# Performance work log

Measured on AMD Instinct MI355X. Metric: run time of the kernel, lower is better.

Reference implementation:

```python
import jax, jax.numpy as jnp
import numpy as np

H = 64  # hidden_dim


def _gru_cell(x, h, W_ih, W_hh, b_ih, b_hh):
    # PyTorch GRU gate order: reset (r), update (z), new (n)
    gx = x @ W_ih.T + b_ih            # [B, 3H]
    gh = h @ W_hh.T + b_hh            # [B, 3H]
    xr, xz, xn = jnp.split(gx, 3, axis=-1)
    hr, hz, hn = jnp.split(gh, 3, axis=-1)
    r = jax.nn.sigmoid(xr + hr)
    z = jax.nn.sigmoid(xz + hz)
    n = jnp.tanh(xn + r * hn)
    return (1.0 - z) * n + z * h


def setup_inputs() -> dict:
    key = jax.random.key(0)
    ks = jax.random.split(key, 11)
    B, T, F_in, A = 1024, 512, 128, 18
    s = 0.05
    return {
        "state": jax.random.normal(ks[0], (B, T, F_in), dtype=jnp.float32),
        "W_ih_l0": jax.random.normal(ks[1], (3 * H, F_in), dtype=jnp.float32) * s,
        "W_hh_l0": jax.random.normal(ks[2], (3 * H, H), dtype=jnp.float32) * s,
        "b_ih_l0": jax.random.normal(ks[3], (3 * H,), dtype=jnp.float32) * s,
        "b_hh_l0": jax.random.normal(ks[4], (3 * H,), dtype=jnp.float32) * s,
        "W_ih_l1": jax.random.normal(ks[5], (3 * H, H), dtype=jnp.float32) * s,
        "W_hh_l1": jax.random.normal(ks[6], (3 * H, H), dtype=jnp.float32) * s,
        "b_ih_l1": jax.random.normal(ks[7], (3 * H,), dtype=jnp.float32) * s,
        "b_hh_l1": jax.random.normal(ks[8], (3 * H,), dtype=jnp.float32) * s,
        "fc3_w": jax.random.normal(ks[9], (A, H), dtype=jnp.float32) * s,
        "fc3_b": jax.random.normal(ks[10], (A,), dtype=jnp.float32) * s,
    }


def reference(state, W_ih_l0, W_hh_l0, b_ih_l0, b_hh_l0,
              W_ih_l1, W_hh_l1, b_ih_l1, b_hh_l1, fc3_w, fc3_b):
    B = state.shape[0]
    h0 = jnp.zeros((B, H), dtype=state.dtype)
    h1 = jnp.zeros((B, H), dtype=state.dtype)
    xs = jnp.swapaxes(state, 0, 1)  # [T, B, F]

    def step(carry, x_t):
        h0, h1 = carry
        h0 = _gru_cell(x_t, h0, W_ih_l0, W_hh_l0, b_ih_l0, b_hh_l0)
        h1 = _gru_cell(h0, h1, W_ih_l1, W_hh_l1, b_ih_l1, b_hh_l1)
        return (h0, h1), None

    (_, h1_last), _ = jax.lax.scan(step, (h0, h1), xs)
    # out[:, -1] of the top GRU layer == final h1; then relu -> linear
    actions = jax.nn.relu(h1_last) @ fc3_w.T + fc3_b
    return actions
```

## Files before the change

kernel.cpp:

```cpp
#include <hip/hip_runtime.h>


#define Tn 512
#define Fn 128
#define Hn 64
#define An 18
#define HS 72

typedef _Float16 half8 __attribute__((ext_vector_type(8)));
typedef float f32x4 __attribute__((ext_vector_type(4)));

#define MFMA(a, b, c) __builtin_amdgcn_mfma_f32_16x16x32_f16((a), (b), (c), 0, 0, 0)

static __device__ __forceinline__ float sigm(float x) {
    return __builtin_amdgcn_rcpf(1.0f + __builtin_amdgcn_exp2f(-1.4426950408889634f * x));
}
static __device__ __forceinline__ float tanh_f(float x) {
    return 2.0f * __builtin_amdgcn_rcpf(1.0f + __builtin_amdgcn_exp2f(-2.8853900817779268f * x)) - 1.0f;
}

__global__ __launch_bounds__(768) void gru_fused(
    const float* __restrict__ state,
    const float* __restrict__ Wih0, const float* __restrict__ Whh0,
    const float* __restrict__ bih0, const float* __restrict__ bhh0,
    const float* __restrict__ Wih1, const float* __restrict__ Whh1,
    const float* __restrict__ bih1, const float* __restrict__ bhh1,
    const float* __restrict__ fcw, const float* __restrict__ fcb,
    float* __restrict__ out)
{
    const int tid  = threadIdx.x;
    const int wv12 = tid >> 6;
    const int lane = tid & 63, c = lane & 15, q = lane >> 4;
    const int wv   = wv12 & 3;
    const int r0   = blockIdx.x * 16;
    const int gc   = wv * 16 + c;
    const int role = (wv12 < 4) ? 0 : (wv12 < 8 ? 1 : 2);

    __shared__ __align__(16) float    gxring[2][4][3][64][4];
    __shared__ __align__(16) _Float16 h0buf[2][16 * HS];
    __shared__ __align__(16) _Float16 h1buf[2][16 * HS];
    __shared__ float fbuf[16 * 64];

    for (int i = tid; i < 2 * 16 * HS; i += 768) {
        (&h0buf[0][0])[i] = (_Float16)0.0f;
        (&h1buf[0][0])[i] = (_Float16)0.0f;
    }

    half8 W[12];
    f32x4 bias0, bias1, bias2, bias3;
    f32x4 xf32[8];
    f32x4 hreg = {0.f, 0.f, 0.f, 0.f};
    const float* srow = state + (size_t)(r0 + c) * (Tn * Fn);

    if (role == 0) {
#pragma unroll
        for (int gsel = 0; gsel < 3; ++gsel) {
            const int g = gsel * 64 + gc;
#pragma unroll
            for (int ks = 0; ks < 4; ++ks) {
                const float* p = Wih0 + g * Fn + ks * 32 + q * 8;
#pragma unroll
                for (int j = 0; j < 8; ++j) W[gsel * 4 + ks][j] = (_Float16)p[j];
            }
        }
        {
            const float b0 = bih0[gc] + bhh0[gc];
            const float b1 = bih0[64 + gc] + bhh0[64 + gc];
            const float b2 = bih0[128 + gc];
            bias0 = (f32x4){b0, b0, b0, b0};
            bias1 = (f32x4){b1, b1, b1, b1};
            bias2 = (f32x4){b2, b2, b2, b2};
        }
#pragma unroll
        for (int ks = 0; ks < 4; ++ks) {
            xf32[2 * ks]     = *(const f32x4*)(srow + ks * 32 + q * 8);
            xf32[2 * ks + 1] = *(const f32x4*)(srow + ks * 32 + q * 8 + 4);
        }
        half8 xf[4];
#pragma unroll
        for (int ks = 0; ks < 4; ++ks)
#pragma unroll
            for (int i = 0; i < 4; ++i) {
                xf[ks][i]     = (_Float16)xf32[2 * ks][i];
                xf[ks][4 + i] = (_Float16)xf32[2 * ks + 1][i];
            }
        f32x4 a0 = bias0, a1 = bias1, a2 = bias2;
#pragma unroll
        for (int ks = 0; ks < 4; ++ks) {
            a0 = MFMA(xf[ks], W[ks], a0);
            a1 = MFMA(xf[ks], W[4 + ks], a1);
            a2 = MFMA(xf[ks], W[8 + ks], a2);
        }
        *(f32x4*)&gxring[0][wv][0][lane][0] = a0;
        *(f32x4*)&gxring[0][wv][1][lane][0] = a1;
        *(f32x4*)&gxring[0][wv][2][lane][0] = a2;
#pragma unroll
        for (int ks = 0; ks < 4; ++ks) {
            xf32[2 * ks]     = *(const f32x4*)(srow + Fn + ks * 32 + q * 8);
            xf32[2 * ks + 1] = *(const f32x4*)(srow + Fn + ks * 32 + q * 8 + 4);
        }
    } else if (role == 1) {
#pragma unroll
        for (int gsel = 0; gsel < 3; ++gsel) {
            const int g = gsel * 64 + gc;
#pragma unroll
            for (int ks = 0; ks < 2; ++ks) {
                const float* p = Whh0 + g * Hn + ks * 32 + q * 8;
#pragma unroll
                for (int j = 0; j < 8; ++j) W[gsel * 2 + ks][j] = (_Float16)p[j];
            }
        }
        const float bhn = bhh0[128 + gc];
        bias3 = (f32x4){bhn, bhn, bhn, bhn};
    } else {
#pragma unroll
        for (int gsel = 0; gsel < 3; ++gsel) {
            const int g = gsel * 64 + gc;
#pragma unroll
            for (int ks = 0; ks < 2; ++ks) {
                const float* pa = Wih1 + g * Hn + ks * 32 + q * 8;
                const float* pb = Whh1 + g * Hn + ks * 32 + q * 8;
#pragma unroll
                for (int j = 0; j < 8; ++j) {
                    W[gsel * 2 + ks][j]     = (_Float16)pa[j];
                    W[6 + gsel * 2 + ks][j] = (_Float16)pb[j];
                }
            }
        }
        const float br = bih1[gc] + bhh1[gc];
        const float bz = bih1[64 + gc] + bhh1[64 + gc];
        const float bxn = bih1[128 + gc];
        const float bhn = bhh1[128 + gc];
        bias0 = (f32x4){br, br, br, br};
        bias1 = (f32x4){bz, bz, bz, bz};
        bias2 = (f32x4){bxn, bxn, bxn, bxn};
        bias3 = (f32x4){bhn, bhn, bhn, bhn};
    }

    const int ardr = c * HS + q * 8;
    const int wrow = (q * 4) * HS + gc;

    for (int t = 0; t <= Tn; ++t) {
        __syncthreads();
        const int pr = (t & 1) ^ 1, pw = t & 1;
        if (role == 0) {
            if (t < Tn - 1) {
                half8 xf[4];
#pragma unroll
                for (int ks = 0; ks < 4; ++ks)
#pragma unroll
                    for (int i = 0; i < 4; ++i) {
                        xf[ks][i]     = (_Float16)xf32[2 * ks][i];
                        xf[ks][4 + i] = (_Float16)xf32[2 * ks + 1][i];
                    }
                const int tnx = (t + 2 < Tn) ? (t + 2) : (Tn - 1);
#pragma unroll
                for (int ks = 0; ks < 4; ++ks) {
                    xf32[2 * ks]     = *(const f32x4*)(srow + (size_t)tnx * Fn + ks * 32 + q * 8);
                    xf32[2 * ks + 1] = *(const f32x4*)(srow + (size_t)tnx * Fn + ks * 32 + q * 8 + 4);
                }
                f32x4 a0 = bias0, a1 = bias1, a2 = bias2;
#pragma unroll
                for (int ks = 0; ks < 4; ++ks) {
                    a0 = MFMA(xf[ks], W[ks], a0);
                    a1 = MFMA(xf[ks], W[4 + ks], a1);
                    a2 = MFMA(xf[ks], W[8 + ks], a2);
                }
                const int slot = (t + 1) & 1;
                *(f32x4*)&gxring[slot][wv][0][lane][0] = a0;
                *(f32x4*)&gxring[slot][wv][1][lane][0] = a1;
                *(f32x4*)&gxring[slot][wv][2][lane][0] = a2;
            }
        } else if (role == 1) {
            if (t < Tn) {
                f32x4 accr  = *(const f32x4*)&gxring[t & 1][wv][0][lane][0];
                f32x4 accz  = *(const f32x4*)&gxring[t & 1][wv][1][lane][0];
                f32x4 accxn = *(const f32x4*)&gxring[t & 1][wv][2][lane][0];
                const half8 hf0 = *(const half8*)&h0buf[pr][ardr];
                const half8 hf1 = *(const half8*)&h0buf[pr][ardr + 32];
                accr = MFMA(hf0, W[0], accr);
                accr = MFMA(hf1, W[1], accr);
                accz = MFMA(hf0, W[2], accz);
                accz = MFMA(hf1, W[3], accz);
                f32x4 acchn = MFMA(hf0, W[4], bias3);
                acchn = MFMA(hf1, W[5], acchn);
#pragma unroll
                for (int i = 0; i < 4; ++i) {
                    const float rg = sigm(accr[i]);
                    const float zg = sigm(accz[i]);
                    const float ng = tanh_f(accxn[i] + rg * acchn[i]);
                    hreg[i] = ng + zg * (hreg[i] - ng);
                }
#pragma unroll
                for (int i = 0; i < 4; ++i) h0buf[pw][wrow + i * HS] = (_Float16)hreg[i];
            }
        } else {
            if (t >= 1) {
                const half8 xf0 = *(const half8*)&h0buf[pr][ardr];
                const half8 xf1 = *(const half8*)&h0buf[pr][ardr + 32];
                const half8 hf0 = *(const half8*)&h1buf[pw][ardr];
                const half8 hf1 = *(const half8*)&h1buf[pw][ardr + 32];
                f32x4 accr = MFMA(xf0, W[0], bias0);
                accr = MFMA(xf1, W[1], accr);
                f32x4 accz = MFMA(xf0, W[2], bias1);
                accz = MFMA(xf1, W[3], accz);
                f32x4 accxn = MFMA(xf0, W[4], bias2);
                accxn = MFMA(xf1, W[5], accxn);
                accr = MFMA(hf0, W[6], accr);
                accr = MFMA(hf1, W[7], accr);
                accz = MFMA(hf0, W[8], accz);
                accz = MFMA(hf1, W[9], accz);
                f32x4 acchn = MFMA(hf0, W[10], bias3);
                acchn = MFMA(hf1, W[11], acchn);
#pragma unroll
                for (int i = 0; i < 4; ++i) {
                    const float rg = sigm(accr[i]);
                    const float zg = sigm(accz[i]);
                    const float ng = tanh_f(accxn[i] + rg * acchn[i]);
                    hreg[i] = ng + zg * (hreg[i] - ng);
                }
#pragma unroll
                for (int i = 0; i < 4; ++i) h1buf[pr][wrow + i * HS] = (_Float16)hreg[i];
            }
        }
    }

    if (role == 2) {
#pragma unroll
        for (int i = 0; i < 4; ++i) fbuf[(q * 4 + i) * 64 + gc] = fmaxf(hreg[i], 0.0f);
    }
    __syncthreads();
    for (int idx = tid; idx < 16 * An; idx += 768) {
        const int row = idx / An, a = idx - row * An;
        float acc = fcb[a];
#pragma unroll 16
        for (int k = 0; k < Hn; ++k) acc += fbuf[row * 64 + k] * fcw[a * Hn + k];
        out[(size_t)(r0 + row) * An + a] = acc;
    }
}

extern "C" void kernel_launch(void* const* d_in, const int* in_sizes, int n_in,
                              void* d_out, int out_size, void* d_ws, size_t ws_size,
                              hipStream_t stream) {
    const float* state = (const float*)d_in[0];
    const float* Wih0  = (const float*)d_in[1];
    const float* Whh0  = (const float*)d_in[2];
    const float* bih0  = (const float*)d_in[3];
    const float* bhh0  = (const float*)d_in[4];
    const float* Wih1  = (const float*)d_in[5];
    const float* Whh1  = (const float*)d_in[6];
    const float* bih1  = (const float*)d_in[7];
    const float* bhh1  = (const float*)d_in[8];
    const float* fcw   = (const float*)d_in[9];
    const float* fcb   = (const float*)d_in[10];
    float* out = (float*)d_out;

    gru_fused<<<64, 768, 0, stream>>>(state, Wih0, Whh0, bih0, bhh0,
                                      Wih1, Whh1, bih1, bhh1, fcw, fcb, out);
}
```

Before: 741.9 us.

## Merge layer-0 input projection into recurrent waves and pre-convert state to fp16

Removes the separate input-projection wave group and its LDS gx ring. Layer-0 waves now compute the x·W_ih and h·W_hh MFMAs together each step, cutting the block from 12 to 8 waves. A pre-pass kernel converts the whole state tensor to fp16 in workspace, so the recurrent loop loads half as many bytes and skips per-step conversion, with prefetch of x two to three steps ahead. The barrier is replaced by an lgkmcnt wait plus s_barrier. This adds a full extra read and write pass over the 256 MB input and more MFMA work on the layer-0 critical path.

```diff
diff --git a/kernel.cpp b/kernel.cpp
--- a/kernel.cpp
+++ b/kernel.cpp
@@ -8,9 +8,11 @@
 #define HS 72
 
 typedef _Float16 half8 __attribute__((ext_vector_type(8)));
+typedef _Float16 half4 __attribute__((ext_vector_type(4)));
 typedef float f32x4 __attribute__((ext_vector_type(4)));
 
 #define MFMA(a, b, c) __builtin_amdgcn_mfma_f32_16x16x32_f16((a), (b), (c), 0, 0, 0)
+#define BAR() asm volatile("s_waitcnt lgkmcnt(0)\n\ts_barrier" ::: "memory")
 
 static __device__ __forceinline__ float sigm(float x) {
     return __builtin_amdgcn_rcpf(1.0f + __builtin_amdgcn_exp2f(-1.4426950408889634f * x));
@@ -19,8 +21,22 @@
     return 2.0f * __builtin_amdgcn_rcpf(1.0f + __builtin_amdgcn_exp2f(-2.8853900817779268f * x)) - 1.0f;
 }
 
-__global__ __launch_bounds__(768) void gru_fused(
-    const float* __restrict__ state,
+__global__ __launch_bounds__(256) void state_to_f16(const float* __restrict__ in,
+                                                    _Float16* __restrict__ out, int n4) {
+    int i = blockIdx.x * blockDim.x + threadIdx.x;
+    const int stride = gridDim.x * blockDim.x;
+    for (; i < n4; i += stride) {
+        f32x4 v = ((const f32x4*)in)[i];
+        half4 h;
+#pragma unroll
+        for (int j = 0; j < 4; ++j) h[j] = (_Float16)v[j];
+        ((half4*)out)[i] = h;
+    }
+}
+
+template <bool XF16>
+__global__ __launch_bounds__(512) void gru_fused2(
+    const float* __restrict__ state, const _Float16* __restrict__ statef16,
     const float* __restrict__ Wih0, const float* __restrict__ Whh0,
     const float* __restrict__ bih0, const float* __restrict__ bhh0,
     const float* __restrict__ Wih1, const float* __restrict__ Whh1,
@@ -29,30 +45,32 @@
     float* __restrict__ out)
 {
     const int tid  = threadIdx.x;
-    const int wv12 = tid >> 6;
+    const int wv8  = tid >> 6;
     const int lane = tid & 63, c = lane & 15, q = lane >> 4;
-    const int wv   = wv12 & 3;
+    const bool isL0 = (wv8 < 4);
+    const int wv   = wv8 & 3;
     const int r0   = blockIdx.x * 16;
     const int gc   = wv * 16 + c;
-    const int role = (wv12 < 4) ? 0 : (wv12 < 8 ? 1 : 2);
-
-    __shared__ __align__(16) float    gxring[2][4][3][64][4];
+
     __shared__ __align__(16) _Float16 h0buf[2][16 * HS];
     __shared__ __align__(16) _Float16 h1buf[2][16 * HS];
     __shared__ float fbuf[16 * 64];
 
-    for (int i = tid; i < 2 * 16 * HS; i += 768) {
+    for (int i = tid; i < 2 * 16 * HS; i += 512) {
         (&h0buf[0][0])[i] = (_Float16)0.0f;
         (&h1buf[0][0])[i] = (_Float16)0.0f;
     }
 
-    half8 W[12];
+    half8 W[18];
     f32x4 bias0, bias1, bias2, bias3;
-    f32x4 xf32[8];
     f32x4 hreg = {0.f, 0.f, 0.f, 0.f};
+    half8 xr[4][4];
+    f32x4 xp[8];
+
+    const _Float16* sx = statef16 + (size_t)(r0 + c) * (Tn * Fn) + q * 8;
     const float* srow = state + (size_t)(r0 + c) * (Tn * Fn);
 
-    if (role == 0) {
+    if (isL0) {
 #pragma unroll
         for (int gsel = 0; gsel < 3; ++gsel) {
             const int g = gsel * 64 + gc;
@@ -62,56 +80,34 @@
 #pragma unroll
                 for (int j = 0; j < 8; ++j) W[gsel * 4 + ks][j] = (_Float16)p[j];
             }
-        }
-        {
-            const float b0 = bih0[gc] + bhh0[gc];
-            const float b1 = bih0[64 + gc] + bhh0[64 + gc];
-            const float b2 = bih0[128 + gc];
-            bias0 = (f32x4){b0, b0, b0, b0};
-            bias1 = (f32x4){b1, b1, b1, b1};
-            bias2 = (f32x4){b2, b2, b2, b2};
-        }
-#pragma unroll
-        for (int ks = 0; ks < 4; ++ks) {
-            xf32[2 * ks]     = *(const f32x4*)(srow + ks * 32 + q * 8);
-            xf32[2 * ks + 1] = *(const f32x4*)(srow + ks * 32 + q * 8 + 4);
-        }
-        half8 xf[4];
-#pragma unroll
-        for (int ks = 0; ks < 4; ++ks)
-#pragma unroll
-            for (int i = 0; i < 4; ++i) {
-                xf[ks][i]     = (_Float16)xf32[2 * ks][i];
-                xf[ks][4 + i] = (_Float16)xf32[2 * ks + 1][i];
-            }
-        f32x4 a0 = bias0, a1 = bias1, a2 = bias2;
-#pragma unroll
-        for (int ks = 0; ks < 4; ++ks) {
-            a0 = MFMA(xf[ks], W[ks], a0);
-            a1 = MFMA(xf[ks], W[4 + ks], a1);
-            a2 = MFMA(xf[ks], W[8 + ks], a2);
-        }
-        *(f32x4*)&gxring[0][wv][0][lane][0] = a0;
-        *(f32x4*)&gxring[0][wv][1][lane][0] = a1;
-        *(f32x4*)&gxring[0][wv][2][lane][0] = a2;
-#pragma unroll
-        for (int ks = 0; ks < 4; ++ks) {
-            xf32[2 * ks]     = *(const f32x4*)(srow + Fn + ks * 32 + q * 8);
-            xf32[2 * ks + 1] = *(const f32x4*)(srow + Fn + ks * 32 + q * 8 + 4);
-        }
-    } else if (role == 1) {
-#pragma unroll
-        for (int gsel = 0; gsel < 3; ++gsel) {
-            const int g = gsel * 64 + gc;
 #pragma unroll
             for (int ks = 0; ks < 2; ++ks) {
                 const float* p = Whh0 + g * Hn + ks * 32 + q * 8;
 #pragma unroll
-                for (int j = 0; j < 8; ++j) W[gsel * 2 + ks][j] = (_Float16)p[j];
-            }
-        }
+                for (int j = 0; j < 8; ++j) W[12 + gsel * 2 + ks][j] = (_Float16)p[j];
+            }
+        }
+        const float br = bih0[gc] + bhh0[gc];
+        const float bz = bih0[64 + gc] + bhh0[64 + gc];
+        const float bxn = bih0[128 + gc];
         const float bhn = bhh0[128 + gc];
+        bias0 = (f32x4){br, br, br, br};
+        bias1 = (f32x4){bz, bz, bz, bz};
+        bias2 = (f32x4){bxn, bxn, bxn, bxn};
         bias3 = (f32x4){bhn, bhn, bhn, bhn};
+        if (XF16) {
+#pragma unroll
+            for (int s = 0; s < 2; ++s)
+#pragma unroll
+                for (int ks = 0; ks < 4; ++ks)
+                    xr[s][ks] = *(const half8*)(sx + (size_t)s * Fn + ks * 32);
+        } else {
+#pragma unroll
+            for (int ks = 0; ks < 4; ++ks) {
+                xp[2 * ks]     = *(const f32x4*)(srow + ks * 32 + q * 8);
+                xp[2 * ks + 1] = *(const f32x4*)(srow + ks * 32 + q * 8 + 4);
+            }
+        }
     } else {
 #pragma unroll
         for (int gsel = 0; gsel < 3; ++gsel) {
@@ -140,50 +136,58 @@
     const int ardr = c * HS + q * 8;
     const int wrow = (q * 4) * HS + gc;
 
-    for (int t = 0; t <= Tn; ++t) {
-        __syncthreads();
-        const int pr = (t & 1) ^ 1, pw = t & 1;
-        if (role == 0) {
-            if (t < Tn - 1) {
-                half8 xf[4];
-#pragma unroll
-                for (int ks = 0; ks < 4; ++ks)
-#pragma unroll
-                    for (int i = 0; i < 4; ++i) {
-                        xf[ks][i]     = (_Float16)xf32[2 * ks][i];
-                        xf[ks][4 + i] = (_Float16)xf32[2 * ks + 1][i];
-                    }
-                const int tnx = (t + 2 < Tn) ? (t + 2) : (Tn - 1);
-#pragma unroll
-                for (int ks = 0; ks < 4; ++ks) {
-                    xf32[2 * ks]     = *(const f32x4*)(srow + (size_t)tnx * Fn + ks * 32 + q * 8);
-                    xf32[2 * ks + 1] = *(const f32x4*)(srow + (size_t)tnx * Fn + ks * 32 + q * 8 + 4);
-                }
-                f32x4 a0 = bias0, a1 = bias1, a2 = bias2;
-#pragma unroll
-                for (int ks = 0; ks < 4; ++ks) {
-                    a0 = MFMA(xf[ks], W[ks], a0);
-                    a1 = MFMA(xf[ks], W[4 + ks], a1);
-                    a2 = MFMA(xf[ks], W[8 + ks], a2);
-                }
-                const int slot = (t + 1) & 1;
-                *(f32x4*)&gxring[slot][wv][0][lane][0] = a0;
-                *(f32x4*)&gxring[slot][wv][1][lane][0] = a1;
-                *(f32x4*)&gxring[slot][wv][2][lane][0] = a2;
-            }
-        } else if (role == 1) {
-            if (t < Tn) {
-                f32x4 accr  = *(const f32x4*)&gxring[t & 1][wv][0][lane][0];
-                f32x4 accz  = *(const f32x4*)&gxring[t & 1][wv][1][lane][0];
-                f32x4 accxn = *(const f32x4*)&gxring[t & 1][wv][2][lane][0];
+    __syncthreads();
+
+    for (int tb = 0; tb < Tn; tb += 4) {
+#pragma unroll
+        for (int k = 0; k < 4; ++k) {
+            const int t = tb + k;
+            const int pr = (t & 1) ^ 1, pw = t & 1;
+            if (isL0) {
                 const half8 hf0 = *(const half8*)&h0buf[pr][ardr];
                 const half8 hf1 = *(const half8*)&h0buf[pr][ardr + 32];
-                accr = MFMA(hf0, W[0], accr);
-                accr = MFMA(hf1, W[1], accr);
-                accz = MFMA(hf0, W[2], accz);
-                accz = MFMA(hf1, W[3], accz);
-                f32x4 acchn = MFMA(hf0, W[4], bias3);
-                acchn = MFMA(hf1, W[5], acchn);
+                half8 xf[4];
+                if (XF16) {
+                    if ((k & 1) == 0) {
+                        const int ta = (t + 2 < Tn) ? t + 2 : Tn - 1;
+                        const int tb2 = (t + 3 < Tn) ? t + 3 : Tn - 1;
+#pragma unroll
+                        for (int ks = 0; ks < 4; ++ks)
+                            xr[(k + 2) & 3][ks] = *(const half8*)(sx + (size_t)ta * Fn + ks * 32);
+#pragma unroll
+                        for (int ks = 0; ks < 4; ++ks)
+                            xr[(k + 3) & 3][ks] = *(const half8*)(sx + (size_t)tb2 * Fn + ks * 32);
+                    }
+#pragma unroll
+                    for (int ks = 0; ks < 4; ++ks) xf[ks] = xr[k][ks];
+                } else {
+#pragma unroll
+                    for (int ks = 0; ks < 4; ++ks)
+#pragma unroll
+                        for (int i = 0; i < 4; ++i) {
+                            xf[ks][i]     = (_Float16)xp[2 * ks][i];
+                            xf[ks][4 + i] = (_Float16)xp[2 * ks + 1][i];
+                        }
+                    const int tnx = (t + 1 < Tn) ? t + 1 : t;
+#pragma unroll
+                    for (int ks = 0; ks < 4; ++ks) {
+                        xp[2 * ks]     = *(const f32x4*)(srow + (size_t)tnx * Fn + ks * 32 + q * 8);
+                        xp[2 * ks + 1] = *(const f32x4*)(srow + (size_t)tnx * Fn + ks * 32 + q * 8 + 4);
+                    }
+                }
+                f32x4 accr = bias0, accz = bias1, accxn = bias2;
+#pragma unroll
+                for (int ks = 0; ks < 4; ++ks) {
+                    accr  = MFMA(xf[ks], W[ks], accr);
+                    accz  = MFMA(xf[ks], W[4 + ks], accz);
+                    accxn = MFMA(xf[ks], W[8 + ks], accxn);
+                }
+                accr = MFMA(hf0, W[12], accr);
+                accr = MFMA(hf1, W[13], accr);
+                accz = MFMA(hf0, W[14], accz);
+                accz = MFMA(hf1, W[15], accz);
+                f32x4 acchn = MFMA(hf0, W[16], bias3);
+                acchn = MFMA(hf1, W[17], acchn);
 #pragma unroll
                 for (int i = 0; i < 4; ++i) {
                     const float rg = sigm(accr[i]);
@@ -193,48 +197,74 @@
                 }
 #pragma unroll
                 for (int i = 0; i < 4; ++i) h0buf[pw][wrow + i * HS] = (_Float16)hreg[i];
-            }
-        } else {
-            if (t >= 1) {
-                const half8 xf0 = *(const half8*)&h0buf[pr][ardr];
-                const half8 xf1 = *(const half8*)&h0buf[pr][ardr + 32];
-                const half8 hf0 = *(const half8*)&h1buf[pw][ardr];
-                const half8 hf1 = *(const half8*)&h1buf[pw][ardr + 32];
-                f32x4 accr = MFMA(xf0, W[0], bias0);
-                accr = MFMA(xf1, W[1], accr);
-                f32x4 accz = MFMA(xf0, W[2], bias1);
-                accz = MFMA(xf1, W[3], accz);
-                f32x4 accxn = MFMA(xf0, W[4], bias2);
-                accxn = MFMA(xf1, W[5], accxn);
-                accr = MFMA(hf0, W[6], accr);
-                accr = MFMA(hf1, W[7], accr);
-                accz = MFMA(hf0, W[8], accz);
-                accz = MFMA(hf1, W[9], accz);
-                f32x4 acchn = MFMA(hf0, W[10], bias3);
-                acchn = MFMA(hf1, W[11], acchn);
-#pragma unroll
-                for (int i = 0; i < 4; ++i) {
-                    const float rg = sigm(accr[i]);
-                    const float zg = sigm(accz[i]);
-                    const float ng = tanh_f(accxn[i] + rg * acchn[i]);
-                    hreg[i] = ng + zg * (hreg[i] - ng);
-                }
-#pragma unroll
-                for (int i = 0; i < 4; ++i) h1buf[pr][wrow + i * HS] = (_Float16)hreg[i];
-            }
-        }
-    }
-
-    if (role == 2) {
+            } else {
+                if (t >= 1) {
+                    const half8 xf0 = *(const half8*)&h0buf[pr][ardr];
+                    const half8 xf1 = *(const half8*)&h0buf[pr][ardr + 32];
+                    const half8 hf0 = *(const half8*)&h1buf[pw][ardr];
+                    const half8 hf1 = *(const half8*)&h1buf[pw][ardr + 32];
+                    f32x4 accr = MFMA(xf0, W[0], bias0);
+                    accr = MFMA(xf1, W[1], accr);
+                    f32x4 accz = MFMA(xf0, W[2], bias1);
+                    accz = MFMA(xf1, W[3], accz);
+                    f32x4 accxn = MFMA(xf0, W[4], bias2);
+                    accxn = MFMA(xf1, W[5], accxn);
+                    accr = MFMA(hf0, W[6], accr);
+                    accr = MFMA(hf1, W[7], accr);
+                    accz = MFMA(hf0, W[8], accz);
+                    accz = MFMA(hf1, W[9], accz);
+                    f32x4 acchn = MFMA(hf0, W[10], bias3);
+                    acchn = MFMA(hf1, W[11], acchn);
+#pragma unroll
+                    for (int i = 0; i < 4; ++i) {
+                        const float rg = sigm(accr[i]);
+                        const float zg = sigm(accz[i]);
+                        const float ng = tanh_f(accxn[i] + rg * acchn[i]);
+                        hreg[i] = ng + zg * (hreg[i] - ng);
+                    }
+#pragma unroll
+                    for (int i = 0; i < 4; ++i) h1buf[pr][wrow + i * HS] = (_Float16)hreg[i];
+                }
+            }
+            BAR();
+        }
+    }
+
+    if (!isL0) {
+        const int t = Tn;
+        const int pr = (t & 1) ^ 1, pw = t & 1;
+        const half8 xf0 = *(const half8*)&h0buf[pr][ardr];
+        const half8 xf1 = *(const half8*)&h0buf[pr][ardr + 32];
+        const half8 hf0 = *(const half8*)&h1buf[pw][ardr];
+        const half8 hf1 = *(const half8*)&h1buf[pw][ardr + 32];
+        f32x4 accr = MFMA(xf0, W[0], bias0);
+        accr = MFMA(xf1, W[1], accr);
+        f32x4 accz = MFMA(xf0, W[2], bias1);
+        accz = MFMA(xf1, W[3], accz);
+        f32x4 accxn = MFMA(xf0, W[4], bias2);
+        accxn = MFMA(xf1, W[5], accxn);
+        accr = MFMA(hf0, W[6], accr);
+        accr = MFMA(hf1, W[7], accr);
+        accz = MFMA(hf0, W[8], accz);
+        accz = MFMA(hf1, W[9], accz);
+        f32x4 acchn = MFMA(hf0, W[10], bias3);
+        acchn = MFMA(hf1, W[11], acchn);
+#pragma unroll
+        for (int i = 0; i < 4; ++i) {
+            const float rg = sigm(accr[i]);
+            const float zg = sigm(accz[i]);
+            const float ng = tanh_f(accxn[i] + rg * acchn[i]);
+            hreg[i] = ng + zg * (hreg[i] - ng);
+        }
 #pragma unroll
         for (int i = 0; i < 4; ++i) fbuf[(q * 4 + i) * 64 + gc] = fmaxf(hreg[i], 0.0f);
     }
     __syncthreads();
-    for (int idx = tid; idx < 16 * An; idx += 768) {
+    for (int idx = tid; idx < 16 * An; idx += 512) {
         const int row = idx / An, a = idx - row * An;
         float acc = fcb[a];
 #pragma unroll 16
-        for (int k = 0; k < Hn; ++k) acc += fbuf[row * 64 + k] * fcw[a * Hn + k];
+        for (int kk = 0; kk < Hn; ++kk) acc += fbuf[row * 64 + kk] * fcw[a * Hn + kk];
         out[(size_t)(r0 + row) * An + a] = acc;
     }
 }
@@ -255,6 +285,15 @@
     const float* fcb   = (const float*)d_in[10];
     float* out = (float*)d_out;
 
-    gru_fused<<<64, 768, 0, stream>>>(state, Wih0, Whh0, bih0, bhh0,
-                                      Wih1, Whh1, bih1, bhh1, fcw, fcb, out);
-}
+    const size_t nstate = (size_t)1024 * Tn * Fn;
+    if (ws_size >= nstate * sizeof(_Float16)) {
+        _Float16* sf16 = (_Float16*)d_ws;
+        state_to_f16<<<2048, 256, 0, stream>>>(state, sf16, (int)(nstate / 4));
+        gru_fused2<true><<<64, 512, 0, stream>>>(state, sf16, Wih0, Whh0, bih0, bhh0,
+                                                 Wih1, Whh1, bih1, bhh1, fcw, fcb, out);
+    } else {
+        gru_fused2<false><<<64, 512, 0, stream>>>(state, (const _Float16*)d_ws,
+                                                  Wih0, Whh0, bih0, bhh0,
+                                                  Wih1, Whh1, bih1, bhh1, fcw, fcb, out);
+    }
+}
```

Result: slower. 790.3 us (+6.5%).
